# Kernel tuning notes

Measured on AMD Instinct MI355X. Metric: run time of the kernel, lower is better.

## Reference

```python
import jax, jax.numpy as jnp
import numpy as np

EPS = 1e-06
QMAX = 127.0  # int8 dynamic quant max magnitude


def setup_inputs() -> dict:
    key = jax.random.key(0)
    k1, k2 = jax.random.split(key)
    B, S, H = 4, 4096, 4096
    hidden_states = jax.random.normal(k1, (B, S, H), dtype=jnp.float32)
    weight = jax.random.uniform(k2, (H,), dtype=jnp.float32, minval=0.5, maxval=1.5)
    return {"hidden_states": hidden_states, "weight": weight}


def reference(hidden_states, weight):
    # RMSNorm in fp32 (matches rms_norm_dynamic_quant which accumulates in fp32)
    x = hidden_states.astype(jnp.float32)
    var = jnp.mean(x * x, axis=-1, keepdims=True)              # [B, S, 1]
    normed = x * jax.lax.rsqrt(var + EPS) * weight             # [B, S, H]
    # Dynamic per-token int8 quantization: scale = max|row| / 127
    absmax = jnp.max(jnp.abs(normed), axis=-1, keepdims=True)  # [B, S, 1]
    rms_scale = absmax / QMAX
    q = jnp.clip(jnp.round(normed / rms_scale), -128.0, 127.0).astype(jnp.int8)
    return q, rms_scale
```

## Files before the change

kernel.cpp:

```cpp
#include <hip/hip_runtime.h>
#include <hip/hip_bf16.h>


constexpr int H = 4096;
constexpr int BLOCK = 256;
constexpr int VPT = H / (BLOCK * 4);

__global__ __launch_bounds__(BLOCK)
void qrmsnorm_kernel(const float* __restrict__ x, const float* __restrict__ w,
                     float* __restrict__ out, float* __restrict__ scale_out) {
    const int row = blockIdx.x;
    const long long base = (long long)row * H;
    const float4* __restrict__ xv = (const float4*)(x + base);
    const float4* __restrict__ wv = (const float4*)w;

    float4 xw[VPT];
    float ss = 0.0f;
    float am = 0.0f;

#pragma unroll
    for (int j = 0; j < VPT; ++j) {
        const int idx = j * BLOCK + threadIdx.x;
        float4 xx = xv[idx];
        float4 ww = wv[idx];
        ss = fmaf(xx.x, xx.x, ss);
        ss = fmaf(xx.y, xx.y, ss);
        ss = fmaf(xx.z, xx.z, ss);
        ss = fmaf(xx.w, xx.w, ss);
        float4 p;
        p.x = xx.x * ww.x; p.y = xx.y * ww.y;
        p.z = xx.z * ww.z; p.w = xx.w * ww.w;
        am = fmaxf(am, fmaxf(fmaxf(fabsf(p.x), fabsf(p.y)),
                             fmaxf(fabsf(p.z), fabsf(p.w))));
        xw[j] = p;
    }

#pragma unroll
    for (int off = 32; off > 0; off >>= 1) {
        ss += __shfl_down(ss, off);
        am = fmaxf(am, __shfl_down(am, off));
    }

    __shared__ float s_ss[BLOCK / 64];
    __shared__ float s_am[BLOCK / 64];
    const int wave = threadIdx.x >> 6;
    const int lane = threadIdx.x & 63;
    if (lane == 0) { s_ss[wave] = ss; s_am[wave] = am; }
    __syncthreads();

    const float tss = s_ss[0] + s_ss[1] + s_ss[2] + s_ss[3];
    const float tam = fmaxf(fmaxf(s_am[0], s_am[1]), fmaxf(s_am[2], s_am[3]));

    const float rstd = rsqrtf(tss * (1.0f / (float)H) + 1e-6f);
    const float inv = (tam > 0.0f) ? (127.0f / tam) : 0.0f;

    float4* __restrict__ ov = (float4*)(out + base);
#pragma unroll
    for (int j = 0; j < VPT; ++j) {
        const int idx = j * BLOCK + threadIdx.x;
        float4 p = xw[j];
        float4 q;
        q.x = fminf(fmaxf(rintf(p.x * inv), -128.0f), 127.0f);
        q.y = fminf(fmaxf(rintf(p.y * inv), -128.0f), 127.0f);
        q.z = fminf(fmaxf(rintf(p.z * inv), -128.0f), 127.0f);
        q.w = fminf(fmaxf(rintf(p.w * inv), -128.0f), 127.0f);
        ov[idx] = q;
    }

    if (threadIdx.x == 0) {
        scale_out[row] = tam * rstd * (1.0f / 127.0f);
    }
}

extern "C" void kernel_launch(void* const* d_in, const int* in_sizes, int n_in,
                              void* d_out, int out_size, void* d_ws, size_t ws_size,
                              hipStream_t stream) {
    const float* x = (const float*)d_in[0];
    const float* w = (const float*)d_in[1];
    float* out = (float*)d_out;

    const int h = in_sizes[1];
    const int rows = in_sizes[0] / h;
    float* scale_out = out + (long long)rows * h;

    qrmsnorm_kernel<<<rows, BLOCK, 0, stream>>>(x, w, out, scale_out);
}
```

Before: 419.7 us.

## Process two rows per block with nontemporal loads/stores and hoisted loads

Each block now handles two rows. All x and weight loads are issued up front, and the weight vector is shared between the two rows. Input loads and output stores use nontemporal builtins to avoid cache pollution on a streaming workload, and the wave reduction switches to xor shuffles. This gives more memory-level parallelism per thread and halves the block count, at the cost of higher register use, and it assumes an even row count.

```diff
diff --git a/kernel.cpp b/kernel.cpp
--- a/kernel.cpp
+++ b/kernel.cpp
@@ -6,69 +6,93 @@
 constexpr int BLOCK = 256;
 constexpr int VPT = H / (BLOCK * 4);
 
+typedef float fx4 __attribute__((ext_vector_type(4)));
+
 __global__ __launch_bounds__(BLOCK)
 void qrmsnorm_kernel(const float* __restrict__ x, const float* __restrict__ w,
                      float* __restrict__ out, float* __restrict__ scale_out) {
-    const int row = blockIdx.x;
-    const long long base = (long long)row * H;
-    const float4* __restrict__ xv = (const float4*)(x + base);
-    const float4* __restrict__ wv = (const float4*)w;
+    const int row0 = blockIdx.x * 2;
+    const int row1 = row0 + 1;
+    const fx4* __restrict__ xv0 = (const fx4*)(x + (long long)row0 * H);
+    const fx4* __restrict__ xv1 = (const fx4*)(x + (long long)row1 * H);
+    const fx4* __restrict__ wv = (const fx4*)w;
 
-    float4 xw[VPT];
-    float ss = 0.0f;
-    float am = 0.0f;
+    fx4 ww[VPT], p0[VPT], p1[VPT];
+    float ss0 = 0.0f, am0 = 0.0f, ss1 = 0.0f, am1 = 0.0f;
 
 #pragma unroll
     for (int j = 0; j < VPT; ++j) {
         const int idx = j * BLOCK + threadIdx.x;
-        float4 xx = xv[idx];
-        float4 ww = wv[idx];
-        ss = fmaf(xx.x, xx.x, ss);
-        ss = fmaf(xx.y, xx.y, ss);
-        ss = fmaf(xx.z, xx.z, ss);
-        ss = fmaf(xx.w, xx.w, ss);
-        float4 p;
-        p.x = xx.x * ww.x; p.y = xx.y * ww.y;
-        p.z = xx.z * ww.z; p.w = xx.w * ww.w;
-        am = fmaxf(am, fmaxf(fmaxf(fabsf(p.x), fabsf(p.y)),
-                             fmaxf(fabsf(p.z), fabsf(p.w))));
-        xw[j] = p;
+        p0[j] = __builtin_nontemporal_load(&xv0[idx]);
+        p1[j] = __builtin_nontemporal_load(&xv1[idx]);
+        ww[j] = wv[idx];
+    }
+
+#pragma unroll
+    for (int j = 0; j < VPT; ++j) {
+        fx4 a = p0[j], b = p1[j], c = ww[j];
+        ss0 = fmaf(a.x, a.x, ss0); ss0 = fmaf(a.y, a.y, ss0);
+        ss0 = fmaf(a.z, a.z, ss0); ss0 = fmaf(a.w, a.w, ss0);
+        ss1 = fmaf(b.x, b.x, ss1); ss1 = fmaf(b.y, b.y, ss1);
+        ss1 = fmaf(b.z, b.z, ss1); ss1 = fmaf(b.w, b.w, ss1);
+        a *= c;
+        b *= c;
+        am0 = fmaxf(am0, fmaxf(fmaxf(fabsf(a.x), fabsf(a.y)),
+                               fmaxf(fabsf(a.z), fabsf(a.w))));
+        am1 = fmaxf(am1, fmaxf(fmaxf(fabsf(b.x), fabsf(b.y)),
+                               fmaxf(fabsf(b.z), fabsf(b.w))));
+        p0[j] = a; p1[j] = b;
     }
 
 #pragma unroll
     for (int off = 32; off > 0; off >>= 1) {
-        ss += __shfl_down(ss, off);
-        am = fmaxf(am, __shfl_down(am, off));
+        ss0 += __shfl_xor(ss0, off);
+        ss1 += __shfl_xor(ss1, off);
+        am0 = fmaxf(am0, __shfl_xor(am0, off));
+        am1 = fmaxf(am1, __shfl_xor(am1, off));
     }
 
-    __shared__ float s_ss[BLOCK / 64];
-    __shared__ float s_am[BLOCK / 64];
+    __shared__ float s_red[4][4];
     const int wave = threadIdx.x >> 6;
-    const int lane = threadIdx.x & 63;
-    if (lane == 0) { s_ss[wave] = ss; s_am[wave] = am; }
+    if ((threadIdx.x & 63) == 0) {
+        s_red[wave][0] = ss0; s_red[wave][1] = am0;
+        s_red[wave][2] = ss1; s_red[wave][3] = am1;
+    }
     __syncthreads();
 
-    const float tss = s_ss[0] + s_ss[1] + s_ss[2] + s_ss[3];
-    const float tam = fmaxf(fmaxf(s_am[0], s_am[1]), fmaxf(s_am[2], s_am[3]));
+    const float tss0 = s_red[0][0] + s_red[1][0] + s_red[2][0] + s_red[3][0];
+    const float tam0 = fmaxf(fmaxf(s_red[0][1], s_red[1][1]),
+                             fmaxf(s_red[2][1], s_red[3][1]));
+    const float tss1 = s_red[0][2] + s_red[1][2] + s_red[2][2] + s_red[3][2];
+    const float tam1 = fmaxf(fmaxf(s_red[0][3], s_red[1][3]),
+                             fmaxf(s_red[2][3], s_red[3][3]));
 
-    const float rstd = rsqrtf(tss * (1.0f / (float)H) + 1e-6f);
-    const float inv = (tam > 0.0f) ? (127.0f / tam) : 0.0f;
+    const float inv0 = (tam0 > 0.0f) ? (127.0f / tam0) : 0.0f;
+    const float inv1 = (tam1 > 0.0f) ? (127.0f / tam1) : 0.0f;
 
-    float4* __restrict__ ov = (float4*)(out + base);
+    fx4* __restrict__ ov0 = (fx4*)(out + (long long)row0 * H);
+    fx4* __restrict__ ov1 = (fx4*)(out + (long long)row1 * H);
 #pragma unroll
     for (int j = 0; j < VPT; ++j) {
         const int idx = j * BLOCK + threadIdx.x;
-        float4 p = xw[j];
-        float4 q;
-        q.x = fminf(fmaxf(rintf(p.x * inv), -128.0f), 127.0f);
-        q.y = fminf(fmaxf(rintf(p.y * inv), -128.0f), 127.0f);
-        q.z = fminf(fmaxf(rintf(p.z * inv), -128.0f), 127.0f);
-        q.w = fminf(fmaxf(rintf(p.w * inv), -128.0f), 127.0f);
-        ov[idx] = q;
+        fx4 a = p0[j], b = p1[j], q;
+        q.x = fminf(fmaxf(rintf(a.x * inv0), -128.0f), 127.0f);
+        q.y = fminf(fmaxf(rintf(a.y * inv0), -128.0f), 127.0f);
+        q.z = fminf(fmaxf(rintf(a.z * inv0), -128.0f), 127.0f);
+        q.w = fminf(fmaxf(rintf(a.w * inv0), -128.0f), 127.0f);
+        __builtin_nontemporal_store(q, &ov0[idx]);
+        q.x = fminf(fmaxf(rintf(b.x * inv1), -128.0f), 127.0f);
+        q.y = fminf(fmaxf(rintf(b.y * inv1), -128.0f), 127.0f);
+        q.z = fminf(fmaxf(rintf(b.z * inv1), -128.0f), 127.0f);
+        q.w = fminf(fmaxf(rintf(b.w * inv1), -128.0f), 127.0f);
+        __builtin_nontemporal_store(q, &ov1[idx]);
     }
 
     if (threadIdx.x == 0) {
-        scale_out[row] = tam * rstd * (1.0f / 127.0f);
+        const float rstd0 = rsqrtf(tss0 * (1.0f / (float)H) + 1e-6f);
+        const float rstd1 = rsqrtf(tss1 * (1.0f / (float)H) + 1e-6f);
+        scale_out[row0] = tam0 * rstd0 * (1.0f / 127.0f);
+        scale_out[row1] = tam1 * rstd1 * (1.0f / 127.0f);
     }
 }
 
@@ -83,5 +107,5 @@
     const int rows = in_sizes[0] / h;
     float* scale_out = out + (long long)rows * h;
 
-    qrmsnorm_kernel<<<rows, BLOCK, 0, stream>>>(x, w, out, scale_out);
+    qrmsnorm_kernel<<<rows / 2, BLOCK, 0, stream>>>(x, w, out, scale_out);
 }
```

After: 415.1 us. About the same (-1.1%).

## Use one wavefront per row with xor-shuffle reduction and nontemporal memory ops

Applied to the files above, without the earlier changes.

Each row is now handled by a single 64-lane wavefront instead of a 256-thread block. Row reductions become a pure xor-shuffle butterfly, which removes the shared-memory exchange and the __syncthreads barrier. Input loads and output stores use nontemporal builtins to avoid polluting the cache with streamed data. In exchange each thread holds 16 float4 values in registers, and occupancy and latency hiding now depend on having many single-wave blocks resident.

```diff
diff --git a/kernel.cpp b/kernel.cpp
--- a/kernel.cpp
+++ b/kernel.cpp
@@ -3,72 +3,57 @@
 
 
 constexpr int H = 4096;
-constexpr int BLOCK = 256;
-constexpr int VPT = H / (BLOCK * 4);
+constexpr int WAVE = 64;
+constexpr int VPT = H / (WAVE * 4);
 
-__global__ __launch_bounds__(BLOCK)
+typedef float fx4 __attribute__((ext_vector_type(4)));
+
+__global__ __launch_bounds__(WAVE)
 void qrmsnorm_kernel(const float* __restrict__ x, const float* __restrict__ w,
                      float* __restrict__ out, float* __restrict__ scale_out) {
     const int row = blockIdx.x;
-    const long long base = (long long)row * H;
-    const float4* __restrict__ xv = (const float4*)(x + base);
-    const float4* __restrict__ wv = (const float4*)w;
+    const fx4* __restrict__ xv = (const fx4*)(x + (long long)row * H);
+    const fx4* __restrict__ wv = (const fx4*)w;
 
-    float4 xw[VPT];
-    float ss = 0.0f;
-    float am = 0.0f;
+    fx4 p[VPT];
+    float ss = 0.0f, am = 0.0f;
 
 #pragma unroll
     for (int j = 0; j < VPT; ++j) {
-        const int idx = j * BLOCK + threadIdx.x;
-        float4 xx = xv[idx];
-        float4 ww = wv[idx];
-        ss = fmaf(xx.x, xx.x, ss);
-        ss = fmaf(xx.y, xx.y, ss);
-        ss = fmaf(xx.z, xx.z, ss);
-        ss = fmaf(xx.w, xx.w, ss);
-        float4 p;
-        p.x = xx.x * ww.x; p.y = xx.y * ww.y;
-        p.z = xx.z * ww.z; p.w = xx.w * ww.w;
-        am = fmaxf(am, fmaxf(fmaxf(fabsf(p.x), fabsf(p.y)),
-                             fmaxf(fabsf(p.z), fabsf(p.w))));
-        xw[j] = p;
+        const int idx = j * WAVE + threadIdx.x;
+        fx4 a = __builtin_nontemporal_load(&xv[idx]);
+        fx4 c = wv[idx];
+        ss = fmaf(a.x, a.x, ss); ss = fmaf(a.y, a.y, ss);
+        ss = fmaf(a.z, a.z, ss); ss = fmaf(a.w, a.w, ss);
+        a *= c;
+        am = fmaxf(am, fmaxf(fmaxf(fabsf(a.x), fabsf(a.y)),
+                             fmaxf(fabsf(a.z), fabsf(a.w))));
+        p[j] = a;
     }
 
 #pragma unroll
     for (int off = 32; off > 0; off >>= 1) {
-        ss += __shfl_down(ss, off);
-        am = fmaxf(am, __shfl_down(am, off));
+        ss += __shfl_xor(ss, off);
+        am = fmaxf(am, __shfl_xor(am, off));
     }
 
-    __shared__ float s_ss[BLOCK / 64];
-    __shared__ float s_am[BLOCK / 64];
-    const int wave = threadIdx.x >> 6;
-    const int lane = threadIdx.x & 63;
-    if (lane == 0) { s_ss[wave] = ss; s_am[wave] = am; }
-    __syncthreads();
+    const float inv = (am > 0.0f) ? (127.0f / am) : 0.0f;
 
-    const float tss = s_ss[0] + s_ss[1] + s_ss[2] + s_ss[3];
-    const float tam = fmaxf(fmaxf(s_am[0], s_am[1]), fmaxf(s_am[2], s_am[3]));
-
-    const float rstd = rsqrtf(tss * (1.0f / (float)H) + 1e-6f);
-    const float inv = (tam > 0.0f) ? (127.0f / tam) : 0.0f;
-
-    float4* __restrict__ ov = (float4*)(out + base);
+    fx4* __restrict__ ov = (fx4*)(out + (long long)row * H);
 #pragma unroll
     for (int j = 0; j < VPT; ++j) {
-        const int idx = j * BLOCK + threadIdx.x;
-        float4 p = xw[j];
-        float4 q;
-        q.x = fminf(fmaxf(rintf(p.x * inv), -128.0f), 127.0f);
-        q.y = fminf(fmaxf(rintf(p.y * inv), -128.0f), 127.0f);
-        q.z = fminf(fmaxf(rintf(p.z * inv), -128.0f), 127.0f);
-        q.w = fminf(fmaxf(rintf(p.w * inv), -128.0f), 127.0f);
-        ov[idx] = q;
+        const int idx = j * WAVE + threadIdx.x;
+        fx4 a = p[j], q;
+        q.x = fminf(fmaxf(rintf(a.x * inv), -128.0f), 127.0f);
+        q.y = fminf(fmaxf(rintf(a.y * inv), -128.0f), 127.0f);
+        q.z = fminf(fmaxf(rintf(a.z * inv), -128.0f), 127.0f);
+        q.w = fminf(fmaxf(rintf(a.w * inv), -128.0f), 127.0f);
+        __builtin_nontemporal_store(q, &ov[idx]);
     }
 
     if (threadIdx.x == 0) {
-        scale_out[row] = tam * rstd * (1.0f / 127.0f);
+        const float rstd = rsqrtf(ss * (1.0f / (float)H) + 1e-6f);
+        scale_out[row] = am * rstd * (1.0f / 127.0f);
     }
 }
 
@@ -83,5 +68,5 @@
     const int rows = in_sizes[0] / h;
     float* scale_out = out + (long long)rows * h;
 
-    qrmsnorm_kernel<<<rows, BLOCK, 0, stream>>>(x, w, out, scale_out);
+    qrmsnorm_kernel<<<rows, WAVE, 0, stream>>>(x, w, out, scale_out);
 }
```

Result: no change. 419.6 us (-0.0%).
